# Optimization experiments

Measured on AMD Instinct MI355X. Metric: run time of the kernel, lower is better.

## Reference

```python
import jax, jax.numpy as jnp
import numpy as np

B, S, D, H = 4, 2048, 1024, 16
HD = D // H  # head_dim = 64


def setup_inputs() -> dict:
    key = jax.random.key(0)
    ks = jax.random.split(key, 5)
    scale = 0.02
    x = jax.random.normal(ks[0], (B, S, D), dtype=jnp.float32)
    Wq = jax.random.normal(ks[1], (D, D), dtype=jnp.float32) * scale
    Wk = jax.random.normal(ks[2], (D, D), dtype=jnp.float32) * scale
    Wv = jax.random.normal(ks[3], (D, D), dtype=jnp.float32) * scale
    Wo = jax.random.normal(ks[4], (D, D), dtype=jnp.float32) * scale
    # causal mask, broadcastable [1,1,S,S]; 0 entries get -10000 like masked_fill
    mask = jnp.tril(jnp.ones((S, S), dtype=jnp.int32))[None, None]
    return {"x": x, "Wq": Wq, "Wk": Wk, "Wv": Wv, "Wo": Wo, "mask": mask}


def reference(x, Wq, Wk, Wv, Wo, mask):
    b, s, _ = x.shape
    # nn.Linear: x @ W.T (no bias)
    q = (x @ Wq.T).reshape(b, s, H, HD).transpose(0, 2, 1, 3)  # [B,H,S,HD]
    k = (x @ Wk.T).reshape(b, s, H, HD).transpose(0, 2, 1, 3)
    v = (x @ Wv.T).reshape(b, s, H, HD).transpose(0, 2, 1, 3)
    attn = jnp.einsum('bhqd,bhkd->bhqk', q, k) / (HD ** 0.5)  # [B,H,S,S]
    attn = jnp.where(mask == 0, jnp.float32(-10000.0), attn)
    attn = jax.nn.softmax(attn, axis=-1)
    out = jnp.einsum('bhqk,bhkd->bhqd', attn, v)  # [B,H,S,HD]
    out = out.transpose(0, 2, 1, 3).reshape(b, s, H * HD)
    return out @ Wo.T
```

## Files before the change

kernel.cpp:

```cpp
#include <hip/hip_runtime.h>

typedef float    f4 __attribute__((ext_vector_type(4)));
typedef _Float16 h8 __attribute__((ext_vector_type(8)));
typedef _Float16 h4 __attribute__((ext_vector_type(4)));
typedef _Float16 h2 __attribute__((ext_vector_type(2)));

#define DEV static __device__ __forceinline__

DEV f4 mfma16(h8 a, h8 b, f4 c) {
  return __builtin_amdgcn_mfma_f32_16x16x32_f16(a, b, c, 0, 0, 0);
}

DEV void gload16(const void* g, void* lds) {
  __builtin_amdgcn_global_load_lds((__attribute__((address_space(1))) void*)g,
                                   (__attribute__((address_space(3))) void*)lds,
                                   16, 0, 0);
}

DEV h2 cvtpk(float a, float b) {
  return __builtin_bit_cast(h2, __builtin_amdgcn_cvt_pkrtz(a, b));
}

__global__ __launch_bounds__(256) void cvt_all(
    const float* __restrict__ x,  const float* __restrict__ wq,
    const float* __restrict__ wk, const float* __restrict__ wv,
    const float* __restrict__ wo,
    _Float16* __restrict__ xb, _Float16* __restrict__ wqkv, _Float16* __restrict__ wob)
{
  int b = blockIdx.x;
  const float* src; _Float16* dst; int i4;
  if      (b < 8192)  { src = x;  dst = xb;                 i4 = b * 256; }
  else if (b < 9216)  { src = wq; dst = wqkv;               i4 = (b - 8192)  * 256; }
  else if (b < 10240) { src = wk; dst = wqkv + (1u << 20);  i4 = (b - 9216)  * 256; }
  else if (b < 11264) { src = wv; dst = wqkv + (2u << 20);  i4 = (b - 10240) * 256; }
  else                { src = wo; dst = wob;                i4 = (b - 11264) * 256; }
  i4 += threadIdx.x;
  f4 v = ((const f4*)src)[i4];
  h4 o;
  o[0] = (_Float16)v[0]; o[1] = (_Float16)v[1];
  o[2] = (_Float16)v[2]; o[3] = (_Float16)v[3];
  ((h4*)dst)[i4] = o;
}

template<int MODE, int MF>
__global__ __launch_bounds__(512) void gemmT(
    const _Float16* __restrict__ A, const _Float16* __restrict__ Bt,
    float* __restrict__ C,
    _Float16* __restrict__ Qo, _Float16* __restrict__ Ko, _Float16* __restrict__ Vo,
    int N, int Nt)
{
  constexpr int ASZ = MF * 16 * 64;
  constexpr int BSZ = 8192;
  constexpr int V1  = (MF == 8) ? 12 : 9;
  constexpr int V2  = (MF == 8) ? 10 : 7;
  constexpr int VL3 = (MF == 8) ? 8 : 6;
  constexpr int VL5 = (MF == 8) ? 4 : 3;
  constexpr int VL6 = (MF == 8) ? 2 : 1;
  __shared__ _Float16 Al[4 * ASZ];
  __shared__ _Float16 Bl[4 * BSZ];

  int bid = blockIdx.x;
  int cpx = gridDim.x >> 3;
  bid = (bid & 7) * cpx + (bid >> 3);
  int tm = bid / Nt, tn = bid - tm * Nt;
  int m0 = tm * (MF * 32), n0 = tn * 256;

  int t = threadIdx.x, w = t >> 6, l = t & 63, lo = l & 15, hi = l >> 4;
  int wm = w >> 2, wn = w & 3;

  int rsc = t >> 3;
  int csrc = ((t & 7) ^ (rsc & 7)) * 8;
  const _Float16 *As[2][2], *Bs[2][2];
  #pragma unroll
  for (int q = 0; q < 2; ++q) {
    if (MF == 8) {
      As[q][0] = A + (size_t)(m0 + q * 64 + rsc) * 1024 + csrc;
      As[q][1] = A + (size_t)(m0 + 128 + q * 64 + rsc) * 1024 + csrc;
    } else {
      As[q][0] = A + (size_t)(m0 + (t >> 8) * 64 + q * 32 + (rsc & 31)) * 1024 + csrc;
      As[q][1] = As[q][0];
    }
    #pragma unroll
    for (int h = 0; h < 2; ++h)
      Bs[q][h] = Bt + (size_t)(n0 + (2 * h + (t >> 8)) * 64 + q * 32 + (rsc & 31)) * 1024 + csrc;
  }
  _Float16* Adst = Al + w * 512;
  _Float16* Bdst = Bl + w * 512;

  int awoff = wm * (MF * 8 * 64) + lo * 64;
  int bwoff = wn * 2048 + lo * 64;
  int s0 = (hi ^ (lo & 7)) * 8;
  int s1 = ((4 + hi) ^ (lo & 7)) * 8;

  f4 acc[MF][4] = {};
  h8 ar[MF / 2][2], br[2][2][2];

#define VMW(n)  asm volatile("s_waitcnt vmcnt(%0)" :: "n"(n) : "memory")
#define BARR    __builtin_amdgcn_s_barrier()
#define LGKM0   do { asm volatile("s_waitcnt lgkmcnt(0)" ::: "memory"); \
                     __builtin_amdgcn_sched_barrier(0); } while (0)
#define STA(BUF, Q, KO) do { \
    gload16(As[Q][0] + (KO), Adst + ((BUF) * 2 + (Q)) * ASZ); \
    if (MF == 8) gload16(As[Q][1] + (KO), Adst + ((BUF) * 2 + (Q)) * ASZ + 4096); \
  } while (0)
#define STB(BUF, QN, KO) do { \
    gload16(Bs[QN][0] + (KO), Bdst + ((BUF) * 2 + (QN)) * BSZ); \
    gload16(Bs[QN][1] + (KO), Bdst + ((BUF) * 2 + (QN)) * BSZ + 4096); \
  } while (0)
#define RDA(BUF, Q) do { \
    const _Float16* p_ = Al + ((BUF) * 2 + (Q)) * ASZ + awoff; \
    _Pragma("unroll") \
    for (int f_ = 0; f_ < MF / 2; ++f_) { \
      ar[f_][0] = *(const h8*)(p_ + f_ * 1024 + s0); \
      ar[f_][1] = *(const h8*)(p_ + f_ * 1024 + s1); } \
  } while (0)
#define RDB(BUF, QN, D) do { \
    const _Float16* p_ = Bl + ((BUF) * 2 + (QN)) * BSZ + bwoff; \
    br[D][0][0] = *(const h8*)(p_ + s0);        br[D][0][1] = *(const h8*)(p_ + s1); \
    br[D][1][0] = *(const h8*)(p_ + 1024 + s0); br[D][1][1] = *(const h8*)(p_ + 1024 + s1); \
  } while (0)
#define MM(MH, D) do { \
    __builtin_amdgcn_s_setprio(1); \
    _Pragma("unroll") \
    for (int f_ = 0; f_ < MF / 2; ++f_) \
      _Pragma("unroll") \
      for (int g_ = 0; g_ < 2; ++g_) { \
        acc[(MH) * (MF / 2) + f_][(D) * 2 + g_] = \
            mfma16(ar[f_][0], br[D][g_][0], acc[(MH) * (MF / 2) + f_][(D) * 2 + g_]); \
        acc[(MH) * (MF / 2) + f_][(D) * 2 + g_] = \
            mfma16(ar[f_][1], br[D][g_][1], acc[(MH) * (MF / 2) + f_][(D) * 2 + g_]); } \
    __builtin_amdgcn_s_setprio(0); \
    __builtin_amdgcn_sched_barrier(0); \
  } while (0)

  STA(0, 0, 0);  STB(0, 0, 0);  STB(0, 1, 0);  STA(0, 1, 0);
  STA(1, 0, 64); STB(1, 0, 64); STB(1, 1, 64); STA(1, 1, 64);

  int kof = 128;
  #pragma unroll 1
  for (int it = 0; it < 7; ++it) {
    VMW(V1); BARR; RDA(0, 0); RDB(0, 0, 0); LGKM0; MM(0, 0);
    VMW(V2); BARR; RDB(0, 1, 1); STA(0, 0, kof); STB(0, 0, kof); LGKM0; MM(0, 1);
    VMW(V1); BARR; RDA(0, 1); STB(0, 1, kof); LGKM0; MM(1, 1);
    BARR; STA(0, 1, kof); MM(1, 0);
    VMW(V1); BARR; RDA(1, 0); RDB(1, 0, 0); LGKM0; MM(0, 0);
    VMW(V2); BARR; RDB(1, 1, 1); STA(1, 0, kof + 64); STB(1, 0, kof + 64); LGKM0; MM(0, 1);
    VMW(V1); BARR; RDA(1, 1); STB(1, 1, kof + 64); LGKM0; MM(1, 1);
    BARR; STA(1, 1, kof + 64); MM(1, 0);
    kof += 128;
  }
  VMW(V1);  BARR; RDA(0, 0); RDB(0, 0, 0); LGKM0; MM(0, 0);
  VMW(V2);  BARR; RDB(0, 1, 1); LGKM0; MM(0, 1);
  VMW(VL3); BARR; RDA(0, 1); LGKM0; MM(1, 1);
  BARR; MM(1, 0);
  VMW(VL5); BARR; RDA(1, 0); RDB(1, 0, 0); LGKM0; MM(0, 0);
  VMW(VL6); BARR; RDB(1, 1, 1); LGKM0; MM(0, 1);
  VMW(0);   BARR; RDA(1, 1); LGKM0; MM(1, 1);
  BARR; MM(1, 0);

#undef VMW
#undef BARR
#undef LGKM0
#undef STA
#undef STB
#undef RDA
#undef RDB
#undef MM

  if (MODE == 0) {
    #pragma unroll
    for (int mi = 0; mi < MF; ++mi)
      #pragma unroll
      for (int nf = 0; nf < 4; ++nf)
        #pragma unroll
        for (int j = 0; j < 4; ++j) {
          int row = m0 + wm * (MF * 16) + mi * 16 + hi * 4 + j;
          int col = n0 + wn * 64 + nf * 16 + lo;
          C[(size_t)row * N + col] = acc[mi][nf][j];
        }
  } else {
    int which = n0 >> 10;
    int cb0 = (n0 & 1023) + wn * 64;
    if (which == 2) {
      #pragma unroll
      for (int mi = 0; mi < MF; ++mi) {
        int row0 = m0 + wm * (MF * 16) + mi * 16 + hi * 4;
        int bb = row0 >> 11, ss0 = row0 & 2047;
        #pragma unroll
        for (int nf = 0; nf < 4; ++nf) {
          int col = cb0 + nf * 16 + lo;
          int hh = col >> 6, hd = col & 63;
          h4 o4;
          o4[0] = (_Float16)acc[mi][nf][0]; o4[1] = (_Float16)acc[mi][nf][1];
          o4[2] = (_Float16)acc[mi][nf][2]; o4[3] = (_Float16)acc[mi][nf][3];
          *(h4*)(Vo + (size_t)(bb * 16 + hh) * 131072 + (size_t)hd * 2048 + ss0) = o4;
        }
      }
    } else {
      _Float16* Dst = (which == 0) ? Qo : Ko;
      float qs = (which == 0) ? 0.1803368801111137f : 1.0f;
      #pragma unroll
      for (int mi = 0; mi < MF; ++mi)
        #pragma unroll
        for (int nf = 0; nf < 4; ++nf)
          #pragma unroll
          for (int j = 0; j < 4; ++j) {
            int row = m0 + wm * (MF * 16) + mi * 16 + hi * 4 + j;
            int col = cb0 + nf * 16 + lo;
            int hh = col >> 6, hd = col & 63;
            int bb = row >> 11, ss = row & 2047;
            Dst[(size_t)(bb * 16 + hh) * 131072 + (size_t)ss * 64 + hd] =
                (_Float16)(acc[mi][nf][j] * qs);
          }
    }
  }
}

__global__ __launch_bounds__(256, 3) void attn_kernel(
    const _Float16* __restrict__ Q, const _Float16* __restrict__ Kb,
    const _Float16* __restrict__ Vb, _Float16* __restrict__ O)
{
  __shared__ _Float16 Kl[2 * 4096];
  __shared__ _Float16 Vl[2 * 4096];
  __shared__ _Float16 Pl[4 * 2048];

  int bid = blockIdx.x;
  int bh = bid & 63, qi = 15 - (bid >> 6);
  int t = threadIdx.x, w = t >> 6, l = t & 63, lo = l & 15, hi = l >> 4;
  const size_t hoff = (size_t)bh * 131072;
  const _Float16* Kg = Kb + hoff;
  const _Float16* Vg = Vb + hoff;
  _Float16* Pw = Pl + w * 2048;
  int bb = bh >> 4, hh = bh & 15;
  int swz = (lo & 7) << 1;

  int rs = t >> 3, cs = t & 7;
  int sw_ = (cs ^ (rs & 7)) * 8;
  int srcK0 = rs * 64 + sw_,   srcK1 = srcK0 + 2048;
  int srcV0 = rs * 2048 + sw_, srcV1 = srcV0 + 65536;
  _Float16* kd0 = Kl + w * 512;
  _Float16* vd0 = Vl + w * 512;

  int koff[4][2], voff[2][4], pwoff[2][4], proff[2][2];
  #pragma unroll
  for (int kf = 0; kf < 4; ++kf) {
    int row = kf * 16 + lo;
    koff[kf][0] = row * 64 + ((hi       ^ (row & 7)) * 8);
    koff[kf][1] = row * 64 + (((4 + hi) ^ (row & 7)) * 8);
  }
  #pragma unroll
  for (int ks = 0; ks < 2; ++ks)
    #pragma unroll
    for (int df = 0; df < 4; ++df) {
      int row = df * 16 + lo;
      voff[ks][df] = row * 64 + ((((ks << 2) | hi) ^ (row & 7)) * 8);
    }
  #pragma unroll
  for (int m = 0; m < 2; ++m) {
    #pragma unroll
    for (int kf = 0; kf < 4; ++kf)
      pwoff[m][kf] = m * 1024 + lo * 64 + ((((kf << 2) | hi) ^ swz) * 4);
    #pragma unroll
    for (int ks = 0; ks < 2; ++ks)
      proff[m][ks] = m * 1024 + lo * 64 + ((((ks << 3) | (hi << 1)) ^ swz) * 4);
  }

  h8 ones;
  #pragma unroll
  for (int e = 0; e < 8; ++e) ones[e] = (_Float16)1.0f;

  int qb = qi * 128 + w * 32;
  const _Float16* Qp = Q + hoff + (size_t)(qb + lo) * 64 + hi * 8;
  h8 qf[2][2];
  qf[0][0] = *(const h8*)(Qp);
  qf[0][1] = *(const h8*)(Qp + 32);
  qf[1][0] = *(const h8*)(Qp + 1024);
  qf[1][1] = *(const h8*)(Qp + 1056);

  f4 acc[2][4] = {};
  float m_run[2] = {-1e30f, -1e30f};
  float l_run[2] = {0.f, 0.f};
  int nkt = 2 * qi + 2;

#define STAGE(buf, kt) do {                                                   \
    const _Float16* Kt_ = Kg + (size_t)(kt) * 4096;                           \
    const _Float16* Vt_ = Vg + (size_t)(kt) * 64;                             \
    gload16(Kt_ + srcK0, kd0 + (buf) * 4096);                                 \
    gload16(Kt_ + srcK1, kd0 + (buf) * 4096 + 2048);                          \
    gload16(Vt_ + srcV0, vd0 + (buf) * 4096);                                 \
    gload16(Vt_ + srcV1, vd0 + (buf) * 4096 + 2048);                          \
  } while (0)

#define ITER(kt, buf) do {                                                    \
    if ((kt) + 1 < nkt) STAGE(buf ^ 1, (kt) + 1);                             \
    const _Float16* Kc = Kl + (buf) * 4096;                                   \
    const _Float16* Vc = Vl + (buf) * 4096;                                   \
    f4 sc[2][4] = {};                                                         \
    __builtin_amdgcn_s_setprio(1);                                            \
    _Pragma("unroll")                                                         \
    for (int kf = 0; kf < 4; ++kf) {                                          \
      h8 k0 = *(const h8*)(Kc + koff[kf][0]);                                 \
      h8 k1 = *(const h8*)(Kc + koff[kf][1]);                                 \
      _Pragma("unroll")                                                       \
      for (int m = 0; m < 2; ++m) {                                           \
        sc[m][kf] = mfma16(k0, qf[m][0], sc[m][kf]);                          \
        sc[m][kf] = mfma16(k1, qf[m][1], sc[m][kf]);                          \
      }                                                                       \
    }                                                                         \
    __builtin_amdgcn_s_setprio(0);                                            \
    if ((kt) >= 2 * qi) {                                                     \
      _Pragma("unroll")                                                       \
      for (int m = 0; m < 2; ++m) {                                           \
        int qg = qb + m * 16 + lo;                                            \
        _Pragma("unroll")                                                     \
        for (int kf = 0; kf < 4; ++kf) {                                      \
          int kgb = (kt) * 64 + kf * 16 + hi * 4;                             \
          _Pragma("unroll")                                                   \
          for (int j = 0; j < 4; ++j)                                         \
            if (kgb + j > qg) sc[m][kf][j] = -1e30f;                          \
        }                                                                     \
      }                                                                       \
    }                                                                         \
    _Pragma("unroll")                                                         \
    for (int m = 0; m < 2; ++m) {                                             \
      f4 m4 = sc[m][0];                                                       \
      _Pragma("unroll")                                                       \
      for (int kf = 1; kf < 4; ++kf) {                                        \
        m4[0] = fmaxf(m4[0], sc[m][kf][0]); m4[1] = fmaxf(m4[1], sc[m][kf][1]);\
        m4[2] = fmaxf(m4[2], sc[m][kf][2]); m4[3] = fmaxf(m4[3], sc[m][kf][3]);\
      }                                                                       \
      float mx = fmaxf(fmaxf(m4[0], m4[1]), fmaxf(m4[2], m4[3]));             \
      if (!__all(mx <= m_run[m] + 8.f)) {           \
        mx = fmaxf(mx, __shfl_xor(mx, 16));                                   \
        mx = fmaxf(mx, __shfl_xor(mx, 32));                                   \
        float mn = fmaxf(m_run[m], mx);                                       \
        float cr = exp2f(m_run[m] - mn);                                      \
        m_run[m] = mn;                                                        \
        l_run[m] *= cr;                                                       \
        _Pragma("unroll")                                                     \
        for (int df = 0; df < 4; ++df) {                                      \
          acc[m][df][0] *= cr; acc[m][df][1] *= cr;                           \
          acc[m][df][2] *= cr; acc[m][df][3] *= cr;                           \
        }                                                                     \
      }                                                                       \
      float mn = m_run[m];                                                    \
      _Pragma("unroll")                                                       \
      for (int kf = 0; kf < 4; ++kf) {                                        \
        h4 pk;                                                                \
        pk.xy = cvtpk(exp2f(sc[m][kf][0] - mn), exp2f(sc[m][kf][1] - mn));    \
        pk.zw = cvtpk(exp2f(sc[m][kf][2] - mn), exp2f(sc[m][kf][3] - mn));    \
        *(h4*)(Pw + pwoff[m][kf]) = pk;                                       \
      }                                                                       \
    }                                                                         \
    __builtin_amdgcn_sched_barrier(0);                                        \
    asm volatile("s_waitcnt lgkmcnt(0)" ::: "memory");                        \
    __builtin_amdgcn_sched_barrier(0);                                        \
    f4 ls[2] = {};                                                            \
    __builtin_amdgcn_s_setprio(1);                                            \
    _Pragma("unroll")                                                         \
    for (int ks = 0; ks < 2; ++ks) {                                          \
      h8 pf[2];                                                               \
      _Pragma("unroll")                                                       \
      for (int m = 0; m < 2; ++m) {                                           \
        pf[m] = *(const h8*)(Pw + proff[m][ks]);                              \
        ls[m] = mfma16(ones, pf[m], ls[m]);                                   \
      }                                                                       \
      _Pragma("unroll")                                                       \
      for (int df = 0; df < 4; ++df) {                                        \
        h8 vf = *(const h8*)(Vc + voff[ks][df]);                              \
        _Pragma("unroll")                                                     \
        for (int m = 0; m < 2; ++m)                                           \
          acc[m][df] = mfma16(vf, pf[m], acc[m][df]);                         \
      }                                                                       \
    }                                                                         \
    __builtin_amdgcn_s_setprio(0);                                            \
    l_run[0] += ls[0][0];                                                     \
    l_run[1] += ls[1][0];                                                     \
    asm volatile("s_waitcnt vmcnt(0)" ::: "memory");                          \
    __syncthreads();                                                          \
  } while (0)

  STAGE(0, 0);
  asm volatile("s_waitcnt vmcnt(0)" ::: "memory");
  __syncthreads();

  for (int kt = 0; kt < nkt; kt += 2) {
    ITER(kt, 0);
    ITER(kt + 1, 1);
  }

  #pragma unroll
  for (int m = 0; m < 2; ++m) {
    float inv = 1.0f / l_run[m];
    int q = qb + m * 16 + lo;
    _Float16* Op = O + ((size_t)(bb * 2048 + q)) * 1024 + hh * 64 + (hi << 2);
    #pragma unroll
    for (int df = 0; df < 4; ++df) {
      h4 o4;
      o4[0] = (_Float16)(acc[m][df][0] * inv);
      o4[1] = (_Float16)(acc[m][df][1] * inv);
      o4[2] = (_Float16)(acc[m][df][2] * inv);
      o4[3] = (_Float16)(acc[m][df][3] * inv);
      *(h4*)(Op + df * 16) = o4;
    }
  }
#undef ITER
#undef STAGE
}

extern "C" void kernel_launch(void* const* d_in, const int* in_sizes, int n_in,
                              void* d_out, int out_size, void* d_ws, size_t ws_size,
                              hipStream_t stream)
{
  const float* x  = (const float*)d_in[0];
  const float* wq = (const float*)d_in[1];
  const float* wk = (const float*)d_in[2];
  const float* wv = (const float*)d_in[3];
  const float* wo = (const float*)d_in[4];

  char* ws = (char*)d_ws;
  _Float16* xb   = (_Float16*)(ws);
  _Float16* wqkv = (_Float16*)(ws + (16u << 20));
  _Float16* wob  = (_Float16*)(ws + (22u << 20));
  _Float16* Qb   = (_Float16*)(ws + (24u << 20));
  _Float16* Kb   = (_Float16*)(ws + (40u << 20));
  _Float16* Vb   = (_Float16*)(ws + (56u << 20));
  _Float16* Ob   = xb;

  cvt_all<<<12288, 256, 0, stream>>>(x, wq, wk, wv, wo, xb, wqkv, wob);
  gemmT<1, 8><<<32 * 12, 512, 0, stream>>>(xb, wqkv, nullptr, Qb, Kb, Vb, 3072, 12);
  attn_kernel<<<1024, 256, 0, stream>>>(Qb, Kb, Vb, Ob);
  gemmT<0, 4><<<64 * 4, 512, 0, stream>>>(Ob, wob, (float*)d_out,
                                          nullptr, nullptr, nullptr, 1024, 4);
}
```

Baseline: 166.2 us.

## Keep softmax probabilities in registers by permuting K rows in LDS

Drops the per-wave LDS round-trip for the P matrix. K rows are now loaded into shared memory in a permuted order, so each lane's QK^T accumulator fragments line up with the B-operand layout the PV MFMA expects. P is then packed to fp16 straight in registers. The causal-mask key index is remapped to match the permuted order. With the P buffer gone, the LDS footprint shrinks and launch bounds rise to 4 blocks per CU, at some risk of register pressure or spilling.

```diff
diff --git a/kernel.cpp b/kernel.cpp
--- a/kernel.cpp
+++ b/kernel.cpp
@@ -4,6 +4,7 @@
 typedef _Float16 h8 __attribute__((ext_vector_type(8)));
 typedef _Float16 h4 __attribute__((ext_vector_type(4)));
 typedef _Float16 h2 __attribute__((ext_vector_type(2)));
+typedef unsigned u4 __attribute__((ext_vector_type(4)));
 
 #define DEV static __device__ __forceinline__
 
@@ -17,8 +18,8 @@
                                    16, 0, 0);
 }
 
-DEV h2 cvtpk(float a, float b) {
-  return __builtin_bit_cast(h2, __builtin_amdgcn_cvt_pkrtz(a, b));
+DEV unsigned cvtpku(float a, float b) {
+  return __builtin_bit_cast(unsigned, __builtin_amdgcn_cvt_pkrtz(a, b));
 }
 
 __global__ __launch_bounds__(256) void cvt_all(
@@ -216,13 +217,12 @@
   }
 }
 
-__global__ __launch_bounds__(256, 3) void attn_kernel(
+__global__ __launch_bounds__(256, 4) void attn_kernel(
     const _Float16* __restrict__ Q, const _Float16* __restrict__ Kb,
     const _Float16* __restrict__ Vb, _Float16* __restrict__ O)
 {
   __shared__ _Float16 Kl[2 * 4096];
   __shared__ _Float16 Vl[2 * 4096];
-  __shared__ _Float16 Pl[4 * 2048];
 
   int bid = blockIdx.x;
   int bh = bid & 63, qi = 15 - (bid >> 6);
@@ -230,18 +230,17 @@
   const size_t hoff = (size_t)bh * 131072;
   const _Float16* Kg = Kb + hoff;
   const _Float16* Vg = Vb + hoff;
-  _Float16* Pw = Pl + w * 2048;
   int bb = bh >> 4, hh = bh & 15;
-  int swz = (lo & 7) << 1;
 
   int rs = t >> 3, cs = t & 7;
   int sw_ = (cs ^ (rs & 7)) * 8;
-  int srcK0 = rs * 64 + sw_,   srcK1 = srcK0 + 2048;
-  int srcV0 = rs * 2048 + sw_, srcV1 = srcV0 + 65536;
+  int sigma = ((rs & 0x1C) << 1) | (rs & 3);
+  int srcK0 = sigma * 64 + sw_, srcK1 = srcK0 + 256;
+  int srcV0 = rs * 2048 + sw_,  srcV1 = srcV0 + 65536;
   _Float16* kd0 = Kl + w * 512;
   _Float16* vd0 = Vl + w * 512;
 
-  int koff[4][2], voff[2][4], pwoff[2][4], proff[2][2];
+  int koff[4][2], voff[2][4];
   #pragma unroll
   for (int kf = 0; kf < 4; ++kf) {
     int row = kf * 16 + lo;
@@ -255,15 +254,6 @@
       int row = df * 16 + lo;
       voff[ks][df] = row * 64 + ((((ks << 2) | hi) ^ (row & 7)) * 8);
     }
-  #pragma unroll
-  for (int m = 0; m < 2; ++m) {
-    #pragma unroll
-    for (int kf = 0; kf < 4; ++kf)
-      pwoff[m][kf] = m * 1024 + lo * 64 + ((((kf << 2) | hi) ^ swz) * 4);
-    #pragma unroll
-    for (int ks = 0; ks < 2; ++ks)
-      proff[m][ks] = m * 1024 + lo * 64 + ((((ks << 3) | (hi << 1)) ^ swz) * 4);
-  }
 
   h8 ones;
   #pragma unroll
@@ -314,7 +304,7 @@
         int qg = qb + m * 16 + lo;                                            \
         _Pragma("unroll")                                                     \
         for (int kf = 0; kf < 4; ++kf) {                                      \
-          int kgb = (kt) * 64 + kf * 16 + hi * 4;                             \
+          int kgb = (kt) * 64 + ((kf & 1) << 5) + ((kf >> 1) << 2) + hi * 8;  \
           _Pragma("unroll")                                                   \
           for (int j = 0; j < 4; ++j)                                         \
             if (kgb + j > qg) sc[m][kf][j] = -1e30f;                          \
@@ -343,28 +333,27 @@
           acc[m][df][2] *= cr; acc[m][df][3] *= cr;                           \
         }                                                                     \
       }                                                                       \
-      float mn = m_run[m];                                                    \
-      _Pragma("unroll")                                                       \
-      for (int kf = 0; kf < 4; ++kf) {                                        \
-        h4 pk;                                                                \
-        pk.xy = cvtpk(exp2f(sc[m][kf][0] - mn), exp2f(sc[m][kf][1] - mn));    \
-        pk.zw = cvtpk(exp2f(sc[m][kf][2] - mn), exp2f(sc[m][kf][3] - mn));    \
-        *(h4*)(Pw + pwoff[m][kf]) = pk;                                       \
-      }                                                                       \
     }                                                                         \
-    __builtin_amdgcn_sched_barrier(0);                                        \
-    asm volatile("s_waitcnt lgkmcnt(0)" ::: "memory");                        \
-    __builtin_amdgcn_sched_barrier(0);                                        \
     f4 ls[2] = {};                                                            \
-    __builtin_amdgcn_s_setprio(1);                                            \
     _Pragma("unroll")                                                         \
     for (int ks = 0; ks < 2; ++ks) {                                          \
       h8 pf[2];                                                               \
       _Pragma("unroll")                                                       \
       for (int m = 0; m < 2; ++m) {                                           \
-        pf[m] = *(const h8*)(Pw + proff[m][ks]);                              \
+        float mn_ = m_run[m];                                                 \
+        u4 tw;                                                                \
+        tw[0] = cvtpku(exp2f(sc[m][ks    ][0] - mn_),                         \
+                       exp2f(sc[m][ks    ][1] - mn_));                        \
+        tw[1] = cvtpku(exp2f(sc[m][ks    ][2] - mn_),                         \
+                       exp2f(sc[m][ks    ][3] - mn_));                        \
+        tw[2] = cvtpku(exp2f(sc[m][2 + ks][0] - mn_),                         \
+                       exp2f(sc[m][2 + ks][1] - mn_));                        \
+        tw[3] = cvtpku(exp2f(sc[m][2 + ks][2] - mn_),                         \
+                       exp2f(sc[m][2 + ks][3] - mn_));                        \
+        pf[m] = __builtin_bit_cast(h8, tw);                                   \
         ls[m] = mfma16(ones, pf[m], ls[m]);                                   \
       }                                                                       \
+      __builtin_amdgcn_s_setprio(1);                                          \
       _Pragma("unroll")                                                       \
       for (int df = 0; df < 4; ++df) {                                        \
         h8 vf = *(const h8*)(Vc + voff[ks][df]);                              \
@@ -372,8 +361,8 @@
         for (int m = 0; m < 2; ++m)                                           \
           acc[m][df] = mfma16(vf, pf[m], acc[m][df]);                         \
       }                                                                       \
+      __builtin_amdgcn_s_setprio(0);                                          \
     }                                                                         \
-    __builtin_amdgcn_s_setprio(0);                                            \
     l_run[0] += ls[0][0];                                                     \
     l_run[1] += ls[1][0];                                                     \
     asm volatile("s_waitcnt vmcnt(0)" ::: "memory");                          \
```

After: 166.3 us. About the same (+0.0%).
